# Optimization experiments

Hardware: AMD Instinct MI355X
Metric: run time of the kernel (lower is better)

Reference implementation:

```python
import jax, jax.numpy as jnp
import numpy as np

B, S, D, H, FF, R, NB = 8, 1024, 768, 12, 3072, 16, 768


def _ln(x, g, b, eps=1e-6):
    m = x.mean(-1, keepdims=True)
    v = jnp.mean((x - m) ** 2, axis=-1, keepdims=True)
    return (x - m) * jax.lax.rsqrt(v + eps) * g + b


def setup_inputs() -> dict:
    key = jax.random.key(0)

    def rn(i, shape, s=0.02):
        return jax.random.normal(jax.random.fold_in(key, i), shape, jnp.float32) * s

    inp = {
        "x": jax.random.normal(jax.random.fold_in(key, 0), (B, S, D), jnp.float32),
        "attn_mask": jnp.zeros((S, S), jnp.float32),
        "norm1_g": jnp.ones((D,), jnp.float32),
        "norm1_b": jnp.zeros((D,), jnp.float32),
        "q_w": rn(1, (D, D)), "q_b": jnp.zeros((D,), jnp.float32),
        "k_w": rn(2, (D, D)), "k_b": jnp.zeros((D,), jnp.float32),
        "v_w": rn(3, (D, D)), "v_b": jnp.zeros((D,), jnp.float32),
        "o_w": rn(4, (D, D)), "o_b": jnp.zeros((D,), jnp.float32),
        "norm2_g": jnp.ones((D,), jnp.float32),
        "norm2_b": jnp.zeros((D,), jnp.float32),
        "fc1_w": rn(5, (FF, D)), "fc1_b": jnp.zeros((FF,), jnp.float32),
        "fc2_w": rn(6, (D, FF)), "fc2_b": jnp.zeros((D,), jnp.float32),
        # shared LoRA (backbone tokens)
        "lora1_A": rn(7, (D, R)), "lora1_B": rn(8, (R, FF)),
        "lora2_A": rn(9, (FF, R)), "lora2_B": rn(10, (R, D)),
        # expert VeRA: frozen shared A/B, per-expert diagonal scaling vectors
        "vera1_A": rn(11, (D, R)), "vera1_B": rn(12, (R, FF)),
        "vera2_A": rn(13, (FF, R)), "vera2_B": rn(14, (R, D)),
        "expert_fc1_d": rn(15, (R,), 1.0), "expert_fc1_b": rn(16, (FF,), 1.0),
        "expert_fc2_d": rn(17, (R,), 1.0), "expert_fc2_b": rn(18, (D,), 1.0),
        "num_backbone_tokens": NB,
    }
    return inp


def reference(x, attn_mask, norm1_g, norm1_b, q_w, q_b, k_w, k_b, v_w, v_b,
              o_w, o_b, norm2_g, norm2_b, fc1_w, fc1_b, fc2_w, fc2_b,
              lora1_A, lora1_B, lora2_A, lora2_B,
              vera1_A, vera1_B, vera2_A, vera2_B,
              expert_fc1_d, expert_fc1_b, expert_fc2_d, expert_fc2_b,
              num_backbone_tokens):
    bsz, seq, dim = x.shape
    hd = dim // H                      # head_dim = 64
    scale = hd ** -0.5
    nb = num_backbone_tokens

    # ---- attention (manual bmm + mask + softmax, eval-mode dropout = identity) ----
    h = _ln(x, norm1_g, norm1_b)
    q = (h @ q_w.T + q_b).reshape(bsz, seq, H, hd)
    k = (h @ k_w.T + k_b).reshape(bsz, seq, H, hd)
    v = (h @ v_w.T + v_b).reshape(bsz, seq, H, hd)
    scores = jnp.einsum('bqhd,bkhd->bhqk', q * scale, k) + attn_mask  # [B,H,S,S]
    probs = jax.nn.softmax(scores, axis=-1)
    ao = jnp.einsum('bhqk,bkhd->bqhd', probs, v).reshape(bsz, seq, dim)
    x = x + (ao @ o_w.T + o_b)

    # ---- MLP with split backbone (shared LoRA) / expert (VeRA) adapters ----
    residual = x
    n2 = _ln(x, norm2_g, norm2_b)
    hid = n2 @ fc1_w.T + fc1_b                                   # [B,S,FF]
    hid_b = hid[:, :nb] + (n2[:, :nb] @ lora1_A) @ lora1_B
    hid_e = hid[:, nb:] + (((n2[:, nb:] @ vera1_A) * expert_fc1_d) @ vera1_B) * expert_fc1_b
    hid = jnp.concatenate([hid_b, hid_e], axis=1)
    hid = jax.nn.gelu(hid)
    out = hid @ fc2_w.T + fc2_b                                  # [B,S,D]
    out_b = out[:, :nb] + (hid[:, :nb] @ lora2_A) @ lora2_B
    out_e = out[:, nb:] + (((hid[:, nb:] @ vera2_A) * expert_fc2_d) @ vera2_B) * expert_fc2_b
    out = jnp.concatenate([out_b, out_e], axis=1)
    return residual + out
```

## Files before the change

### kernel.cpp

```cpp
#include <hip/hip_runtime.h>
#include <stdint.h>

#define B_  8
#define S_  1024
#define D_  768
#define H_  12
#define HD_ 64
#define FF_ 3072
#define M_  (B_*S_)
#define R_  16
#define QLD 2304
#define KBLK 128

typedef unsigned short u16;
typedef short s16x8 __attribute__((ext_vector_type(8)));
typedef float fx4  __attribute__((ext_vector_type(4)));

__device__ __forceinline__ float b2f(u16 u) {
  union { unsigned int i; float f; } c; c.i = ((unsigned int)u) << 16; return c.f;
}
__device__ __forceinline__ u16 f2b(float f) {
  union { float f; unsigned int i; } c; c.f = f;
  unsigned int x = c.i;
  x += 0x7FFFu + ((x >> 16) & 1u);
  return (u16)(x >> 16);
}
__device__ __forceinline__ float gelu_f(float x) {
  float u = 0.7978845608028654f * (x + 0.044715f * x * x * x);
  float e = __expf(2.f * u);
  float t = 1.f - 2.f / (e + 1.f);
  return 0.5f * x * (1.f + t);
}
__device__ __forceinline__ void gload16(const u16* gsrc, u16* ldst) {
  __builtin_amdgcn_global_load_lds(
      (__attribute__((address_space(1))) void*)(gsrc),
      (__attribute__((address_space(3))) void*)(ldst), 16, 0, 0);
}

__global__ __launch_bounds__(256)
void cvt_all(const float* __restrict__ q_w, const float* __restrict__ k_w,
             const float* __restrict__ v_w, const float* __restrict__ o_w,
             const float* __restrict__ fc1_w, const float* __restrict__ fc2_w,
             u16* __restrict__ wqkv, u16* __restrict__ wo,
             u16* __restrict__ wfc1, u16* __restrict__ wfc2)
{
  const int i = blockIdx.x * 256 + threadIdx.x;
  const int q1  = D_ * D_ / 4;
  const int fd4 = FF_ * D_ / 4;
  const float* s; u16* d; int j;
  if      (i <     q1)       { s = q_w;   d = wqkv;            j = i; }
  else if (i < 2 * q1)       { s = k_w;   d = wqkv + D_*D_;    j = i - q1; }
  else if (i < 3 * q1)       { s = v_w;   d = wqkv + 2*D_*D_;  j = i - 2*q1; }
  else if (i < 4 * q1)       { s = o_w;   d = wo;              j = i - 3*q1; }
  else if (i < 4 * q1 + fd4) { s = fc1_w; d = wfc1;            j = i - 4*q1; }
  else                       { s = fc2_w; d = wfc2;            j = i - 4*q1 - fd4; }
  const float4 f = ((const float4*)s)[j];
  ushort4 o4; o4.x = f2b(f.x); o4.y = f2b(f.y); o4.z = f2b(f.z); o4.w = f2b(f.w);
  ((ushort4*)d)[j] = o4;
}

__global__ __launch_bounds__(256)
void prep_all(const float* __restrict__ q_bv, const float* __restrict__ k_bv,
              const float* __restrict__ v_bv, float* __restrict__ qkvb,
              const float* __restrict__ lora1B, const float* __restrict__ vera1B,
              const float* __restrict__ e1b, u16* __restrict__ up1L, u16* __restrict__ up1V,
              const float* __restrict__ lora2B, const float* __restrict__ vera2B,
              const float* __restrict__ e2b, u16* __restrict__ up2L, u16* __restrict__ up2V,
              const float* __restrict__ lora2A, const float* __restrict__ vera2A,
              u16* __restrict__ a2tL, u16* __restrict__ a2tV)
{
  const int f = blockIdx.x * 256 + threadIdx.x;
  if (f < QLD)
    qkvb[f] = (f < D_) ? q_bv[f] : (f < 2 * D_) ? k_bv[f - D_] : v_bv[f - 2 * D_];
  {
    const float ev = e1b[f];
    #pragma unroll
    for (int r = 0; r < 16; ++r) {
      up1L[(size_t)f * 32 + r] = f2b(lora1B[(size_t)r * FF_ + f]);
      up1V[(size_t)f * 32 + r] = f2b(vera1B[(size_t)r * FF_ + f] * ev);
      up1L[(size_t)f * 32 + 16 + r] = 0;
      up1V[(size_t)f * 32 + 16 + r] = 0;
    }
  }
  {
    const float4* apl = (const float4*)(lora2A + (size_t)f * 16);
    const float4* apv = (const float4*)(vera2A + (size_t)f * 16);
    #pragma unroll
    for (int q4 = 0; q4 < 4; ++q4) {
      const float4 l4 = apl[q4], v4 = apv[q4];
      a2tL[(size_t)(q4*4+0) * FF_ + f] = f2b(l4.x);
      a2tL[(size_t)(q4*4+1) * FF_ + f] = f2b(l4.y);
      a2tL[(size_t)(q4*4+2) * FF_ + f] = f2b(l4.z);
      a2tL[(size_t)(q4*4+3) * FF_ + f] = f2b(l4.w);
      a2tV[(size_t)(q4*4+0) * FF_ + f] = f2b(v4.x);
      a2tV[(size_t)(q4*4+1) * FF_ + f] = f2b(v4.y);
      a2tV[(size_t)(q4*4+2) * FF_ + f] = f2b(v4.z);
      a2tV[(size_t)(q4*4+3) * FF_ + f] = f2b(v4.w);
    }
  }
  if (f < D_) {
    const float ev = e2b[f];
    #pragma unroll
    for (int r = 0; r < 16; ++r) {
      up2L[(size_t)f * 32 + r] = f2b(lora2B[(size_t)r * D_ + f]);
      up2V[(size_t)f * 32 + r] = f2b(vera2B[(size_t)r * D_ + f] * ev);
      up2L[(size_t)f * 32 + 16 + r] = 0;
      up2V[(size_t)f * 32 + 16 + r] = 0;
    }
  }
}

template<bool ADD>
__global__ __launch_bounds__(256)
void ln_k(const float* __restrict__ x, const u16* __restrict__ add,
          const float* __restrict__ g, const float* __restrict__ beta,
          u16* __restrict__ outb, float* __restrict__ xsum,
          const float* __restrict__ Alora, const float* __restrict__ Avera,
          const float* __restrict__ dvec, u16* __restrict__ tmp1b,
          const int* __restrict__ nbp)
{
  const int row = blockIdx.x;
  const size_t base = (size_t)row * D_;
  float v0[3]; float s = 0.f, sq = 0.f;
  #pragma unroll
  for (int i = 0; i < 3; ++i) {
    const int d = threadIdx.x + i * 256;
    float val = x[base + d];
    if (ADD) { val += b2f(add[base + d]); xsum[base + d] = val; }
    v0[i] = val; s += val; sq += val * val;
  }
  #pragma unroll
  for (int mm = 32; mm >= 1; mm >>= 1) { s += __shfl_xor(s, mm); sq += __shfl_xor(sq, mm); }
  __shared__ float ss[4], s2[4];
  if ((threadIdx.x & 63) == 0) { ss[threadIdx.x >> 6] = s; s2[threadIdx.x >> 6] = sq; }
  __syncthreads();
  s  = ss[0] + ss[1] + ss[2] + ss[3];
  sq = s2[0] + s2[1] + s2[2] + s2[3];
  const float mean = s * (1.f / D_);
  const float var  = sq * (1.f / D_) - mean * mean;
  const float rs   = rsqrtf(var + 1e-6f);
  float nv[3];
  #pragma unroll
  for (int i = 0; i < 3; ++i) {
    const int d = threadIdx.x + i * 256;
    nv[i] = (v0[i] - mean) * rs * g[d] + beta[d];
    outb[base + d] = f2b(nv[i]);
  }

  if (ADD) {
    const int nb = *nbp;
    const bool ex = (row % S_) >= nb;
    const float* Am = ex ? Avera : Alora;
    float p[16];
    #pragma unroll
    for (int r = 0; r < 16; ++r) p[r] = 0.f;
    #pragma unroll
    for (int i = 0; i < 3; ++i) {
      const int d = threadIdx.x + i * 256;
      const float4* ap = (const float4*)(Am + (size_t)d * R_);
      const float4 a0 = ap[0], a1 = ap[1], a2 = ap[2], a3 = ap[3];
      const float vv = nv[i];
      p[0]  += vv * a0.x; p[1]  += vv * a0.y; p[2]  += vv * a0.z; p[3]  += vv * a0.w;
      p[4]  += vv * a1.x; p[5]  += vv * a1.y; p[6]  += vv * a1.z; p[7]  += vv * a1.w;
      p[8]  += vv * a2.x; p[9]  += vv * a2.y; p[10] += vv * a2.z; p[11] += vv * a2.w;
      p[12] += vv * a3.x; p[13] += vv * a3.y; p[14] += vv * a3.z; p[15] += vv * a3.w;
    }
    #pragma unroll
    for (int st = 1; st < 16; st <<= 1)
      #pragma unroll
      for (int r = 0; r < 16; ++r) p[r] += __shfl_xor(p[r], st);
    __shared__ float sred[16][16];
    const int grp = threadIdx.x >> 4;
    if ((threadIdx.x & 15) == 0) {
      #pragma unroll
      for (int r = 0; r < 16; ++r) sred[grp][r] = p[r];
    }
    __syncthreads();
    if (threadIdx.x < 16) {
      float v = 0.f;
      #pragma unroll
      for (int gg = 0; gg < 16; ++gg) v += sred[gg][threadIdx.x];
      if (ex) v *= dvec[threadIdx.x];
      tmp1b[(size_t)row * 32 + threadIdx.x] = f2b(v);
      tmp1b[(size_t)row * 32 + 16 + threadIdx.x] = 0;
    }
  }
}

template<int MODE>
__global__ __launch_bounds__(256)
void gemm_bt(const u16* __restrict__ A, const u16* __restrict__ W,
             const float* __restrict__ bias, u16* __restrict__ Cb,
             float* __restrict__ Cf, const float* __restrict__ resid,
             const u16* __restrict__ Aad, const u16* __restrict__ BadL,
             const u16* __restrict__ BadV, const int* __restrict__ nbp,
             int M, int N, int K)
{
  __shared__ u16 As[2][128 * 32];
  __shared__ u16 Bs[2][128 * 32];
  const int tid   = threadIdx.x;
  const int lane  = tid & 63;
  const int wid   = tid >> 6;
  const int wr    = wid >> 1;
  const int wc    = wid & 1;
  const int lr    = lane & 15;
  const int lk    = (lane >> 4) << 3;
  const int gn    = N >> 7;
  const int nwg   = (M >> 7) * gn;
  const int chunk = nwg >> 3;
  const int lin   = blockIdx.x;
  const int swz   = (lin & 7) * chunk + (lin >> 3);
  const int m0    = (swz / gn) * 128;
  const int n0    = (swz % gn) * 128;
  const int kg    = (tid & 3) * 8;
  const int row_a = tid >> 2;

  const int nst = K >> 5;
  const int tot = (MODE >= 1) ? nst + 1 : nst;
  const u16* Bad = nullptr;
  if (MODE >= 1) Bad = ((m0 % S_) >= *nbp) ? BadV : BadL;

  const u16* arow = A + (size_t)(m0 + row_a) * K + kg;
  const u16* wrow = W + (size_t)(n0 + row_a) * K + kg;
  const size_t half_a = (size_t)64 * K;

  fx4 acc[4][4];
  const fx4 zero = {0.f, 0.f, 0.f, 0.f};
  #pragma unroll
  for (int i = 0; i < 4; ++i)
    #pragma unroll
    for (int j = 0; j < 4; ++j) acc[i][j] = zero;

  gload16(arow,          &As[0][tid * 8]);
  gload16(arow + half_a, &As[0][(256 + tid) * 8]);
  gload16(wrow,          &Bs[0][tid * 8]);
  gload16(wrow + half_a, &Bs[0][(256 + tid) * 8]);
  __syncthreads();

  for (int t = 0; t < tot; ++t) {
    const int cur = t & 1;
    if (t + 1 < tot) {
      const int nxt = cur ^ 1;
      if (MODE >= 1 && t + 1 == nst) {
        gload16(Aad + (size_t)(m0 + row_a) * 32 + kg,      &As[nxt][tid * 8]);
        gload16(Aad + (size_t)(m0 + 64 + row_a) * 32 + kg, &As[nxt][(256 + tid) * 8]);
        gload16(Bad + (size_t)(n0 + row_a) * 32 + kg,      &Bs[nxt][tid * 8]);
        gload16(Bad + (size_t)(n0 + 64 + row_a) * 32 + kg, &Bs[nxt][(256 + tid) * 8]);
      } else {
        const size_t ko = (size_t)(t + 1) * 32;
        gload16(arow + ko,          &As[nxt][tid * 8]);
        gload16(arow + ko + half_a, &As[nxt][(256 + tid) * 8]);
        gload16(wrow + ko,          &Bs[nxt][tid * 8]);
        gload16(wrow + ko + half_a, &Bs[nxt][(256 + tid) * 8]);
      }
    }
    s16x8 av[4], bv[4];
    #pragma unroll
    for (int i = 0; i < 4; ++i)
      av[i] = *(const s16x8*)&As[cur][(wr * 64 + i * 16 + lr) * 32 + lk];
    #pragma unroll
    for (int j = 0; j < 4; ++j)
      bv[j] = *(const s16x8*)&Bs[cur][(wc * 64 + j * 16 + lr) * 32 + lk];
    __builtin_amdgcn_s_setprio(1);
    #pragma unroll
    for (int i = 0; i < 4; ++i)
      #pragma unroll
      for (int j = 0; j < 4; ++j)
        acc[i][j] = __builtin_amdgcn_mfma_f32_16x16x32_bf16(av[i], bv[j], acc[i][j], 0, 0, 0);
    __builtin_amdgcn_s_setprio(0);
    __syncthreads();
  }

  const int rb = (lane >> 4) * 4;
  #pragma unroll
  for (int j = 0; j < 4; ++j) {
    const int col = n0 + wc * 64 + j * 16 + lr;
    const float bj = bias ? bias[col] : 0.f;
    #pragma unroll
    for (int i = 0; i < 4; ++i) {
      const int row = m0 + wr * 64 + i * 16 + rb;
      #pragma unroll
      for (int r = 0; r < 4; ++r) {
        const float val = acc[i][j][r] + bj;
        const size_t idx = (size_t)(row + r) * N + col;
        if (MODE == 1)      Cb[idx] = f2b(gelu_f(val));
        else if (MODE == 2) Cf[idx] = resid[idx] + val;
        else                Cb[idx] = f2b(val);
      }
    }
  }
}

__global__ __launch_bounds__(256)
void downproj(const u16* __restrict__ hid, const u16* __restrict__ A2tL,
              const u16* __restrict__ A2tV, float* __restrict__ part,
              const int* __restrict__ nbp)
{
  __shared__ u16 As[2][128 * 32];
  __shared__ u16 Bs[2][16 * 32];
  const int tid  = threadIdx.x;
  const int lane = tid & 63;
  const int w    = tid >> 6;
  const int lr   = lane & 15;
  const int lk   = (lane >> 4) << 3;
  const int m0   = blockIdx.x * 128;
  const int kb   = blockIdx.y * (FF_ / 8);
  const int nb   = *nbp;
  const u16* A2t = ((m0 % S_) >= nb) ? A2tV : A2tL;
  const int kg    = (tid & 3) * 8;
  const int row_a = tid >> 2;

  const u16* hrow = hid + (size_t)(m0 + row_a) * FF_ + kb + kg;
  const size_t half_h = (size_t)64 * FF_;
  const u16* brow = A2t + (size_t)(tid >> 2) * FF_ + kb + kg;

  const fx4 zero = {0.f, 0.f, 0.f, 0.f};
  fx4 acc[2]; acc[0] = zero; acc[1] = zero;

  const int nst = (FF_ / 8) >> 5;
  gload16(hrow,          &As[0][tid * 8]);
  gload16(hrow + half_h, &As[0][(256 + tid) * 8]);
  if (tid < 64) gload16(brow, &Bs[0][tid * 8]);
  __syncthreads();

  for (int t = 0; t < nst; ++t) {
    const int cur = t & 1;
    if (t + 1 < nst) {
      const int nxt = cur ^ 1;
      const size_t ko = (size_t)(t + 1) * 32;
      gload16(hrow + ko,          &As[nxt][tid * 8]);
      gload16(hrow + ko + half_h, &As[nxt][(256 + tid) * 8]);
      if (tid < 64) gload16(brow + ko, &Bs[nxt][tid * 8]);
    }
    s16x8 bv = *(const s16x8*)&Bs[cur][lr * 32 + lk];
    #pragma unroll
    for (int i = 0; i < 2; ++i) {
      s16x8 av = *(const s16x8*)&As[cur][(w * 32 + i * 16 + lr) * 32 + lk];
      acc[i] = __builtin_amdgcn_mfma_f32_16x16x32_bf16(av, bv, acc[i], 0, 0, 0);
    }
    __syncthreads();
  }

  const int rb = (lane >> 4) * 4;
  #pragma unroll
  for (int i = 0; i < 2; ++i)
    #pragma unroll
    for (int r = 0; r < 4; ++r)
      part[(size_t)blockIdx.y * M_ * 16 +
           (size_t)(m0 + w * 32 + i * 16 + rb + r) * 16 + lr] = acc[i][r];
}

__global__ __launch_bounds__(256)
void reduce_dp(const float* __restrict__ part, const float* __restrict__ d2,
               u16* __restrict__ tmp2b, const int* __restrict__ nbp)
{
  const int idx = blockIdx.x * 256 + threadIdx.x;
  const int m = idx >> 4, r = idx & 15;
  const int nb = *nbp;
  float s = 0.f;
  #pragma unroll
  for (int ks = 0; ks < 8; ++ks) s += part[(size_t)ks * M_ * 16 + idx];
  if ((m % S_) >= nb) s *= d2[r];
  tmp2b[(size_t)m * 32 + r] = f2b(s);
  tmp2b[(size_t)m * 32 + 16 + r] = 0;
}

__global__ __launch_bounds__(256)
void attn_mfma(const u16* __restrict__ qkv, const float* __restrict__ mask,
               u16* __restrict__ o)
{
  __shared__ u16 Kl[2][128 * 64];
  __shared__ u16 Vt[2][64 * 128];
  __shared__ uint32_t Pl[4][1024];

  const int tid  = threadIdx.x;
  const int lane = tid & 63;
  const int wq   = tid >> 6;
  const int lr   = lane & 15;
  const int hi   = lane >> 4;
  const int lin = blockIdx.x;
  const int vsw = (lin & 7) * 192 + (lin >> 3);
  const int qb  = vsw & 15;
  const int bh  = vsw >> 4;
  const int b    = bh / H_;
  const int h    = bh % H_;
  const size_t tok0 = (size_t)b * S_ + (size_t)qb * 64;
  const size_t colh = (size_t)h * HD_;

  const int va  = tid >> 3;
  const int vc8 = (tid & 7) * 8;
  u16* qstage = (u16*)&Pl[0][0];

  #pragma unroll
  for (int u = 0; u < 2; ++u) {
    const int li = u * 256 + tid;
    const int r  = li >> 3;
    const int cb = ((li & 7) ^ (r & 7)) * 8;
    gload16(qkv + (tok0 + r) * QLD + colh + cb, &qstage[li * 8]);
  }
  {
    const size_t ktok = (size_t)b * S_;
    #pragma unroll
    for (int u = 0; u < 4; ++u) {
      const int li = u * 256 + tid;
      const int r  = li >> 3;
      const int cb = ((li & 7) ^ (r & 7)) * 8;
      gload16(qkv + (ktok + r) * QLD + D_ + colh + cb, &Kl[0][li * 8]);
    }
    const u16* vp = qkv + (ktok + 4 * va) * QLD + 2 * D_ + colh + vc8;
    s16x8 w0 = *(const s16x8*)vp;
    s16x8 w1 = *(const s16x8*)(vp + QLD);
    s16x8 w2 = *(const s16x8*)(vp + 2 * QLD);
    s16x8 w3 = *(const s16x8*)(vp + 3 * QLD);
    #pragma unroll
    for (int jj = 0; jj < 8; ++jj) {
      const int d  = vc8 + jj;
      const int sw = ((d & 7) ^ ((d >> 3) & 7)) << 3;
      const int cp = (4 * va) ^ sw;
      *(uint32_t*)&Vt[0][d * 128 + cp] =
          (uint32_t)(u16)w0[jj] | ((uint32_t)(u16)w1[jj] << 16);
      *(uint32_t*)&Vt[0][d * 128 + cp + 2] =
          (uint32_t)(u16)w2[jj] | ((uint32_t)(u16)w3[jj] << 16);
    }
  }
  __syncthreads();

  s16x8 qa[2];
  {
    const int qrow = wq * 16 + lr;
    #pragma unroll
    for (int ks = 0; ks < 2; ++ks)
      qa[ks] = *(const s16x8*)&qstage[qrow * 64 + ((ks * 32 + hi * 8) ^ ((qrow & 7) << 3))];
  }
  __syncthreads();

  const fx4 zero = {0.f, 0.f, 0.f, 0.f};
  fx4 oacc[4];
  #pragma unroll
  for (int dj = 0; dj < 4; ++dj) oacc[dj] = zero;
  float mreg = -3.0e38f, lreg = 0.f;

  const int NT = S_ / KBLK;
  for (int kt = 0; kt < NT; ++kt) {
    const int cur = kt & 1;
    const int nxt = cur ^ 1;

    s16x8 w0, w1, w2, w3;
    if (kt + 1 < NT) {
      const size_t ktokn = (size_t)b * S_ + (size_t)(kt + 1) * KBLK;
      #pragma unroll
      for (int u = 0; u < 4; ++u) {
        const int li = u * 256 + tid;
        const int r  = li >> 3;
        const int cb = ((li & 7) ^ (r & 7)) * 8;
        gload16(qkv + (ktokn + r) * QLD + D_ + colh + cb, &Kl[nxt][li * 8]);
      }
      const u16* vp = qkv + (ktokn + 4 * va) * QLD + 2 * D_ + colh + vc8;
      w0 = *(const s16x8*)vp;
      w1 = *(const s16x8*)(vp + QLD);
      w2 = *(const s16x8*)(vp + 2 * QLD);
      w3 = *(const s16x8*)(vp + 3 * QLD);
    }

    float val[8][4];
    #pragma unroll
    for (int jh = 0; jh < 2; ++jh) {
      s16x8 kb2[4][2];
      #pragma unroll
      for (int j = 0; j < 4; ++j) {
        const int n = (jh * 4 + j) * 16 + lr;
        #pragma unroll
        for (int ks = 0; ks < 2; ++ks)
          kb2[j][ks] = *(const s16x8*)&Kl[cur][n * 64 + ((ks * 32 + hi * 8) ^ ((n & 7) << 3))];
      }
      fx4 m4[4];
      {
        const float* mp = mask + (size_t)(qb * 64 + wq * 16 + lr) * S_
                        + (size_t)kt * KBLK + jh * 64 + 4 * hi;
        #pragma unroll
        for (int j = 0; j < 4; ++j)
          m4[j] = *(const fx4*)(mp + j * 16);
      }
      fx4 sf[4];
      #pragma unroll
      for (int j = 0; j < 4; ++j) sf[j] = zero;
      __builtin_amdgcn_s_setprio(1);
      #pragma unroll
      for (int ks = 0; ks < 2; ++ks)
        #pragma unroll
        for (int j = 0; j < 4; ++j)
          sf[j] = __builtin_amdgcn_mfma_f32_16x16x32_bf16(kb2[j][ks], qa[ks], sf[j], 0, 0, 0);
      __builtin_amdgcn_s_setprio(0);
      #pragma unroll
      for (int j = 0; j < 4; ++j)
        #pragma unroll
        for (int r = 0; r < 4; ++r)
          val[jh * 4 + j][r] = sf[j][r] * 0.125f + m4[j][r];
    }

    {
      float mk[8];
      #pragma unroll
      for (int kg = 0; kg < 8; ++kg)
        mk[kg] = fmaxf(fmaxf(val[kg][0], val[kg][1]), fmaxf(val[kg][2], val[kg][3]));
      float mx = fmaxf(fmaxf(fmaxf(mk[0], mk[1]), fmaxf(mk[2], mk[3])),
                       fmaxf(fmaxf(mk[4], mk[5]), fmaxf(mk[6], mk[7])));
      mx = fmaxf(mx, __shfl_xor(mx, 16));
      mx = fmaxf(mx, __shfl_xor(mx, 32));
      const float mn  = fmaxf(mreg, mx);
      const float fac = __expf(mreg - mn);
      mreg = mn;
      float sk[8];
      #pragma unroll
      for (int kg = 0; kg < 8; ++kg) {
        #pragma unroll
        for (int r = 0; r < 4; ++r) val[kg][r] = __expf(val[kg][r] - mn);
        sk[kg] = (val[kg][0] + val[kg][1]) + (val[kg][2] + val[kg][3]);
      }
      float rs = ((sk[0] + sk[1]) + (sk[2] + sk[3])) + ((sk[4] + sk[5]) + (sk[6] + sk[7]));
      rs += __shfl_xor(rs, 16);
      rs += __shfl_xor(rs, 32);
      lreg = lreg * fac + rs;
      float facr[4];
      #pragma unroll
      for (int r = 0; r < 4; ++r) facr[r] = __shfl(fac, hi * 4 + r);
      #pragma unroll
      for (int dj = 0; dj < 4; ++dj)
        #pragma unroll
        for (int r = 0; r < 4; ++r) oacc[dj][r] *= facr[r];
    }

    {
      uint32_t* prow = &Pl[wq][lr * 64];
      #pragma unroll
      for (int kg = 0; kg < 8; ++kg) {
        const uint32_t p0 = __builtin_amdgcn_perm(
            __float_as_uint(val[kg][1]), __float_as_uint(val[kg][0]), 0x07060302u);
        const uint32_t p1 = __builtin_amdgcn_perm(
            __float_as_uint(val[kg][3]), __float_as_uint(val[kg][2]), 0x07060302u);
        const int i0 = (8 * kg + 2 * hi) ^ ((lr & 7) << 3);
        uint2 pk; pk.x = p0; pk.y = p1;
        *(uint2*)&prow[i0] = pk;
      }
    }

    if (kt + 1 < NT) {
      #pragma unroll
      for (int jj = 0; jj < 8; ++jj) {
        const int d  = vc8 + jj;
        const int sw = ((d & 7) ^ ((d >> 3) & 7)) << 3;
        const int cp = (4 * va) ^ sw;
        *(uint32_t*)&Vt[nxt][d * 128 + cp] =
            (uint32_t)(u16)w0[jj] | ((uint32_t)(u16)w1[jj] << 16);
        *(uint32_t*)&Vt[nxt][d * 128 + cp + 2] =
            (uint32_t)(u16)w2[jj] | ((uint32_t)(u16)w3[jj] << 16);
      }
    }

    #pragma unroll
    for (int ks = 0; ks < 4; ++ks) {
      const int pbase = (16 * ks + 4 * hi) ^ ((lr & 7) << 3);
      s16x8 pa = *(const s16x8*)&Pl[wq][lr * 64 + pbase];
      s16x8 bv2[4];
      #pragma unroll
      for (int dj = 0; dj < 4; ++dj) {
        const int n  = dj * 16 + lr;
        const int sw = ((n & 7) ^ ((n >> 3) & 7)) << 3;
        bv2[dj] = *(const s16x8*)&Vt[cur][n * 128 + ((ks * 32 + hi * 8) ^ sw)];
      }
      __builtin_amdgcn_s_setprio(1);
      #pragma unroll
      for (int dj = 0; dj < 4; ++dj)
        oacc[dj] = __builtin_amdgcn_mfma_f32_16x16x32_bf16(pa, bv2[dj], oacc[dj], 0, 0, 0);
      __builtin_amdgcn_s_setprio(0);
    }

    __syncthreads();
  }

  {
    const float linv = 1.f / lreg;
    float invr[4];
    #pragma unroll
    for (int r = 0; r < 4; ++r) invr[r] = __shfl(linv, hi * 4 + r);
    #pragma unroll
    for (int r = 0; r < 4; ++r) {
      const size_t grow = (tok0 + wq * 16 + hi * 4 + r) * D_ + colh;
      #pragma unroll
      for (int dj = 0; dj < 4; ++dj)
        o[grow + dj * 16 + lr] = f2b(oacc[dj][r] * invr[r]);
    }
  }
}

extern "C" void kernel_launch(void* const* d_in, const int* in_sizes, int n_in,
                              void* d_out, int out_size, void* d_ws, size_t ws_size,
                              hipStream_t stream)
{
  const float* x      = (const float*)d_in[0];
  const float* mask   = (const float*)d_in[1];
  const float* n1g    = (const float*)d_in[2];
  const float* n1b    = (const float*)d_in[3];
  const float* q_w    = (const float*)d_in[4];
  const float* q_bv   = (const float*)d_in[5];
  const float* k_w    = (const float*)d_in[6];
  const float* k_bv   = (const float*)d_in[7];
  const float* v_w    = (const float*)d_in[8];
  const float* v_bv   = (const float*)d_in[9];
  const float* o_w    = (const float*)d_in[10];
  const float* o_bv   = (const float*)d_in[11];
  const float* n2g    = (const float*)d_in[12];
  const float* n2b    = (const float*)d_in[13];
  const float* fc1_w  = (const float*)d_in[14];
  const float* fc1_bv = (const float*)d_in[15];
  const float* fc2_w  = (const float*)d_in[16];
  const float* fc2_bv = (const float*)d_in[17];
  const float* lora1A = (const float*)d_in[18];
  const float* lora1B = (const float*)d_in[19];
  const float* lora2A = (const float*)d_in[20];
  const float* lora2B = (const float*)d_in[21];
  const float* vera1A = (const float*)d_in[22];
  const float* vera1B = (const float*)d_in[23];
  const float* vera2A = (const float*)d_in[24];
  const float* vera2B = (const float*)d_in[25];
  const float* e1d    = (const float*)d_in[26];
  const float* e1b    = (const float*)d_in[27];
  const float* e2d    = (const float*)d_in[28];
  const float* e2b    = (const float*)d_in[29];
  const int*   nbp    = (const int*)d_in[30];

  char* wsb = (char*)d_ws;
  u16* h1    = (u16*)wsb; wsb += (size_t)M_ * D_ * 2;
  u16* qkv   = (u16*)wsb; wsb += (size_t)M_ * QLD * 2;
  u16* attno = (u16*)wsb; wsb += (size_t)M_ * D_ * 2;
  u16* oproj = (u16*)wsb; wsb += (size_t)M_ * D_ * 2;
  u16* n2    = (u16*)wsb; wsb += (size_t)M_ * D_ * 2;
  u16* wqkv  = (u16*)wsb; wsb += (size_t)QLD * D_ * 2;
  u16* wo    = (u16*)wsb; wsb += (size_t)D_ * D_ * 2;
  u16* wfc1  = (u16*)wsb; wsb += (size_t)FF_ * D_ * 2;
  u16* wfc2  = (u16*)wsb; wsb += (size_t)D_ * FF_ * 2;
  u16* tmp1b = (u16*)wsb; wsb += (size_t)M_ * 32 * 2;
  u16* tmp2b = (u16*)wsb; wsb += (size_t)M_ * 32 * 2;
  u16* up1L  = (u16*)wsb; wsb += (size_t)FF_ * 32 * 2;
  u16* up1V  = (u16*)wsb; wsb += (size_t)FF_ * 32 * 2;
  u16* up2L  = (u16*)wsb; wsb += (size_t)D_ * 32 * 2;
  u16* up2V  = (u16*)wsb; wsb += (size_t)D_ * 32 * 2;
  u16* a2tL  = (u16*)wsb; wsb += (size_t)16 * FF_ * 2;
  u16* a2tV  = (u16*)wsb; wsb += (size_t)16 * FF_ * 2;
  float* qkvb = (float*)wsb; wsb += (size_t)QLD * 4;
  float* part = (float*)wsb; wsb += (size_t)8 * M_ * 16 * 4;
  u16* hidb = h1;

  const int totq = (4 * D_ * D_ + 2 * FF_ * D_) / 4;
  cvt_all<<<totq / 256, 256, 0, stream>>>(q_w, k_w, v_w, o_w, fc1_w, fc2_w,
                                          wqkv, wo, wfc1, wfc2);
  prep_all<<<FF_ / 256, 256, 0, stream>>>(q_bv, k_bv, v_bv, qkvb,
                                          lora1B, vera1B, e1b, up1L, up1V,
                                          lora2B, vera2B, e2b, up2L, up2V,
                                          lora2A, vera2A, a2tL, a2tV);

  ln_k<false><<<M_, 256, 0, stream>>>(x, nullptr, n1g, n1b, h1, nullptr,
                                      nullptr, nullptr, nullptr, nullptr, nullptr);
  gemm_bt<0><<<(M_/128) * (QLD/128), 256, 0, stream>>>(
      h1, wqkv, qkvb, qkv, nullptr, nullptr, nullptr, nullptr, nullptr, nullptr,
      M_, QLD, D_);
  attn_mfma<<<(S_/64) * (B_*H_), 256, 0, stream>>>(qkv, mask, attno);
  gemm_bt<0><<<(M_/128) * (D_/128), 256, 0, stream>>>(
      attno, wo, o_bv, oproj, nullptr, nullptr, nullptr, nullptr, nullptr, nullptr,
      M_, D_, D_);

  ln_k<true><<<M_, 256, 0, stream>>>(x, oproj, n2g, n2b, n2, (float*)d_out,
                                     lora1A, vera1A, e1d, tmp1b, nbp);

  gemm_bt<1><<<(M_/128) * (FF_/128), 256, 0, stream>>>(
      n2, wfc1, fc1_bv, hidb, nullptr, nullptr, tmp1b, up1L, up1V, nbp,
      M_, FF_, D_);

  downproj<<<dim3(M_/128, 8), 256, 0, stream>>>(hidb, a2tL, a2tV, part, nbp);
  reduce_dp<<<M_*16/256, 256, 0, stream>>>(part, e2d, tmp2b, nbp);

  gemm_bt<2><<<(M_/128) * (D_/128), 256, 0, stream>>>(
      hidb, wfc2, fc2_bv, nullptr, (float*)d_out, (const float*)d_out,
      tmp2b, up2L, up2V, nbp, M_, D_, FF_);
}
```

Baseline: 369.4 us.

## Enlarge attention query block to 128 with 8 waves and register-shuffled P

Raises the attention kernel to 8 waves per block covering 128 queries, so each K/V tile loaded into LDS is shared by twice as many query rows and per-thread global load work halves. It also drops the per-wave P staging buffer in LDS: probabilities are packed to bf16 with v_cvt_pk_bf16_f32 and rearranged into the MFMA A-operand layout through lane shuffles. The Q staging reuses the second K buffer. In exchange it adds many cross-lane shuffles, changes the rounding of P from truncation to round-to-nearest, and raises register pressure under the 512-thread launch bound.

Measured after the change: 396.9 us. 1.07x slower.

```diff
diff --git a/kernel.cpp b/kernel.cpp
--- a/kernel.cpp
+++ b/kernel.cpp
@@ -11,6 +11,7 @@
 #define R_  16
 #define QLD 2304
 #define KBLK 128
+#define QBLK 128
 
 typedef unsigned short u16;
 typedef short s16x8 __attribute__((ext_vector_type(8)));
@@ -35,6 +36,11 @@
   __builtin_amdgcn_global_load_lds(
       (__attribute__((address_space(1))) void*)(gsrc),
       (__attribute__((address_space(3))) void*)(ldst), 16, 0, 0);
+}
+__device__ __forceinline__ uint32_t cvtpk(float lo, float hi_) {
+  uint32_t r;
+  asm volatile("v_cvt_pk_bf16_f32 %0, %1, %2" : "=v"(r) : "v"(lo), "v"(hi_));
+  return r;
 }
 
 __global__ __launch_bounds__(256)
@@ -365,72 +371,68 @@
   tmp2b[(size_t)m * 32 + 16 + r] = 0;
 }
 
-__global__ __launch_bounds__(256)
+__global__ __launch_bounds__(512, 4)
 void attn_mfma(const u16* __restrict__ qkv, const float* __restrict__ mask,
                u16* __restrict__ o)
 {
-  __shared__ u16 Kl[2][128 * 64];
-  __shared__ u16 Vt[2][64 * 128];
-  __shared__ uint32_t Pl[4][1024];
+  __shared__ u16 Kl[2][KBLK * 64];
+  __shared__ u16 Vt[2][64 * KBLK];
 
   const int tid  = threadIdx.x;
   const int lane = tid & 63;
-  const int wq   = tid >> 6;
+  const int w    = tid >> 6;
   const int lr   = lane & 15;
   const int hi   = lane >> 4;
   const int lin = blockIdx.x;
-  const int vsw = (lin & 7) * 192 + (lin >> 3);
-  const int qb  = vsw & 15;
-  const int bh  = vsw >> 4;
+  const int vsw = (lin & 7) * 96 + (lin >> 3);
+  const int qb  = vsw & 7;
+  const int bh  = vsw >> 3;
   const int b    = bh / H_;
   const int h    = bh % H_;
-  const size_t tok0 = (size_t)b * S_ + (size_t)qb * 64;
+  const size_t tok0 = (size_t)b * S_ + (size_t)qb * QBLK;
   const size_t colh = (size_t)h * HD_;
 
   const int va  = tid >> 3;
   const int vc8 = (tid & 7) * 8;
-  u16* qstage = (u16*)&Pl[0][0];
+  const int SA  = 32 * (hi & 1) + lr;
+  const int SB  = SA + 16;
 
   #pragma unroll
   for (int u = 0; u < 2; ++u) {
-    const int li = u * 256 + tid;
+    const int li = u * 512 + tid;
     const int r  = li >> 3;
     const int cb = ((li & 7) ^ (r & 7)) * 8;
-    gload16(qkv + (tok0 + r) * QLD + colh + cb, &qstage[li * 8]);
+    gload16(qkv + (tok0 + r) * QLD + colh + cb, &Kl[1][li * 8]);
   }
   {
     const size_t ktok = (size_t)b * S_;
     #pragma unroll
-    for (int u = 0; u < 4; ++u) {
-      const int li = u * 256 + tid;
+    for (int u = 0; u < 2; ++u) {
+      const int li = u * 512 + tid;
       const int r  = li >> 3;
       const int cb = ((li & 7) ^ (r & 7)) * 8;
       gload16(qkv + (ktok + r) * QLD + D_ + colh + cb, &Kl[0][li * 8]);
     }
-    const u16* vp = qkv + (ktok + 4 * va) * QLD + 2 * D_ + colh + vc8;
+    const u16* vp = qkv + (ktok + 2 * va) * QLD + 2 * D_ + colh + vc8;
     s16x8 w0 = *(const s16x8*)vp;
     s16x8 w1 = *(const s16x8*)(vp + QLD);
-    s16x8 w2 = *(const s16x8*)(vp + 2 * QLD);
-    s16x8 w3 = *(const s16x8*)(vp + 3 * QLD);
     #pragma unroll
     for (int jj = 0; jj < 8; ++jj) {
       const int d  = vc8 + jj;
       const int sw = ((d & 7) ^ ((d >> 3) & 7)) << 3;
-      const int cp = (4 * va) ^ sw;
-      *(uint32_t*)&Vt[0][d * 128 + cp] =
+      const int cp = (2 * va) ^ sw;
+      *(uint32_t*)&Vt[0][d * KBLK + cp] =
           (uint32_t)(u16)w0[jj] | ((uint32_t)(u16)w1[jj] << 16);
-      *(uint32_t*)&Vt[0][d * 128 + cp + 2] =
-          (uint32_t)(u16)w2[jj] | ((uint32_t)(u16)w3[jj] << 16);
     }
   }
   __syncthreads();
 
   s16x8 qa[2];
   {
-    const int qrow = wq * 16 + lr;
+    const int qrow = w * 16 + lr;
     #pragma unroll
     for (int ks = 0; ks < 2; ++ks)
-      qa[ks] = *(const s16x8*)&qstage[qrow * 64 + ((ks * 32 + hi * 8) ^ ((qrow & 7) << 3))];
+      qa[ks] = *(const s16x8*)&Kl[1][qrow * 64 + ((ks * 32 + hi * 8) ^ ((qrow & 7) << 3))];
   }
   __syncthreads();
 
@@ -445,21 +447,19 @@
     const int cur = kt & 1;
     const int nxt = cur ^ 1;
 
-    s16x8 w0, w1, w2, w3;
+    s16x8 w0, w1;
     if (kt + 1 < NT) {
       const size_t ktokn = (size_t)b * S_ + (size_t)(kt + 1) * KBLK;
       #pragma unroll
-      for (int u = 0; u < 4; ++u) {
-        const int li = u * 256 + tid;
+      for (int u = 0; u < 2; ++u) {
+        const int li = u * 512 + tid;
         const int r  = li >> 3;
         const int cb = ((li & 7) ^ (r & 7)) * 8;
         gload16(qkv + (ktokn + r) * QLD + D_ + colh + cb, &Kl[nxt][li * 8]);
       }
-      const u16* vp = qkv + (ktokn + 4 * va) * QLD + 2 * D_ + colh + vc8;
+      const u16* vp = qkv + (ktokn + 2 * va) * QLD + 2 * D_ + colh + vc8;
       w0 = *(const s16x8*)vp;
       w1 = *(const s16x8*)(vp + QLD);
-      w2 = *(const s16x8*)(vp + 2 * QLD);
-      w3 = *(const s16x8*)(vp + 3 * QLD);
     }
 
     float val[8][4];
@@ -475,7 +475,7 @@
       }
       fx4 m4[4];
       {
-        const float* mp = mask + (size_t)(qb * 64 + wq * 16 + lr) * S_
+        const float* mp = mask + (size_t)(qb * QBLK + w * 16 + lr) * S_
                         + (size_t)kt * KBLK + jh * 64 + 4 * hi;
         #pragma unroll
         for (int j = 0; j < 4; ++j)
@@ -530,18 +530,32 @@
         for (int r = 0; r < 4; ++r) oacc[dj][r] *= facr[r];
     }
 
-    {
-      uint32_t* prow = &Pl[wq][lr * 64];
-      #pragma unroll
-      for (int kg = 0; kg < 8; ++kg) {
-        const uint32_t p0 = __builtin_amdgcn_perm(
-            __float_as_uint(val[kg][1]), __float_as_uint(val[kg][0]), 0x07060302u);
-        const uint32_t p1 = __builtin_amdgcn_perm(
-            __float_as_uint(val[kg][3]), __float_as_uint(val[kg][2]), 0x07060302u);
-        const int i0 = (8 * kg + 2 * hi) ^ ((lr & 7) << 3);
-        uint2 pk; pk.x = p0; pk.y = p1;
-        *(uint2*)&prow[i0] = pk;
-      }
+    uint32_t c[8][2];
+    #pragma unroll
+    for (int kg = 0; kg < 8; ++kg) {
+      c[kg][0] = cvtpk(val[kg][0], val[kg][1]);
+      c[kg][1] = cvtpk(val[kg][2], val[kg][3]);
+    }
+    const bool upk = hi >= 2;
+    s16x8 pa[4];
+    #pragma unroll
+    for (int ks = 0; ks < 4; ++ks) {
+      const uint32_t e0a = (uint32_t)__shfl((int)c[2*ks][0],   SA);
+      const uint32_t e0b = (uint32_t)__shfl((int)c[2*ks+1][0], SA);
+      const uint32_t e1a = (uint32_t)__shfl((int)c[2*ks][1],   SA);
+      const uint32_t e1b_ = (uint32_t)__shfl((int)c[2*ks+1][1], SA);
+      const uint32_t e2a = (uint32_t)__shfl((int)c[2*ks][0],   SB);
+      const uint32_t e2b_ = (uint32_t)__shfl((int)c[2*ks+1][0], SB);
+      const uint32_t e3a = (uint32_t)__shfl((int)c[2*ks][1],   SB);
+      const uint32_t e3b = (uint32_t)__shfl((int)c[2*ks+1][1], SB);
+      uint32_t pv[4];
+      pv[0] = upk ? e0b  : e0a;
+      pv[1] = upk ? e1b_ : e1a;
+      pv[2] = upk ? e2b_ : e2a;
+      pv[3] = upk ? e3b  : e3a;
+      union { uint32_t u[4]; s16x8 v; } cvt;
+      cvt.u[0] = pv[0]; cvt.u[1] = pv[1]; cvt.u[2] = pv[2]; cvt.u[3] = pv[3];
+      pa[ks] = cvt.v;
     }
 
     if (kt + 1 < NT) {
@@ -549,29 +563,25 @@
       for (int jj = 0; jj < 8; ++jj) {
         const int d  = vc8 + jj;
         const int sw = ((d & 7) ^ ((d >> 3) & 7)) << 3;
-        const int cp = (4 * va) ^ sw;
-        *(uint32_t*)&Vt[nxt][d * 128 + cp] =
+        const int cp = (2 * va) ^ sw;
+        *(uint32_t*)&Vt[nxt][d * KBLK + cp] =
             (uint32_t)(u16)w0[jj] | ((uint32_t)(u16)w1[jj] << 16);
-        *(uint32_t*)&Vt[nxt][d * 128 + cp + 2] =
-            (uint32_t)(u16)w2[jj] | ((uint32_t)(u16)w3[jj] << 16);
       }
     }
 
     #pragma unroll
     for (int ks = 0; ks < 4; ++ks) {
-      const int pbase = (16 * ks + 4 * hi) ^ ((lr & 7) << 3);
-      s16x8 pa = *(const s16x8*)&Pl[wq][lr * 64 + pbase];
       s16x8 bv2[4];
       #pragma unroll
       for (int dj = 0; dj < 4; ++dj) {
         const int n  = dj * 16 + lr;
         const int sw = ((n & 7) ^ ((n >> 3) & 7)) << 3;
-        bv2[dj] = *(const s16x8*)&Vt[cur][n * 128 + ((ks * 32 + hi * 8) ^ sw)];
+        bv2[dj] = *(const s16x8*)&Vt[cur][n * KBLK + ((ks * 32 + hi * 8) ^ sw)];
       }
       __builtin_amdgcn_s_setprio(1);
       #pragma unroll
       for (int dj = 0; dj < 4; ++dj)
-        oacc[dj] = __builtin_amdgcn_mfma_f32_16x16x32_bf16(pa, bv2[dj], oacc[dj], 0, 0, 0);
+        oacc[dj] = __builtin_amdgcn_mfma_f32_16x16x32_bf16(pa[ks], bv2[dj], oacc[dj], 0, 0, 0);
       __builtin_amdgcn_s_setprio(0);
     }
 
@@ -585,7 +595,7 @@
     for (int r = 0; r < 4; ++r) invr[r] = __shfl(linv, hi * 4 + r);
     #pragma unroll
     for (int r = 0; r < 4; ++r) {
-      const size_t grow = (tok0 + wq * 16 + hi * 4 + r) * D_ + colh;
+      const size_t grow = (tok0 + w * 16 + hi * 4 + r) * D_ + colh;
       #pragma unroll
       for (int dj = 0; dj < 4; ++dj)
         o[grow + dj * 16 + lr] = f2b(oacc[dj][r] * invr[r]);
@@ -664,7 +674,7 @@
   gemm_bt<0><<<(M_/128) * (QLD/128), 256, 0, stream>>>(
       h1, wqkv, qkvb, qkv, nullptr, nullptr, nullptr, nullptr, nullptr, nullptr,
       M_, QLD, D_);
-  attn_mfma<<<(S_/64) * (B_*H_), 256, 0, stream>>>(qkv, mask, attno);
+  attn_mfma<<<(S_/QBLK) * (B_*H_), 512, 0, stream>>>(qkv, mask, attno);
   gemm_bt<0><<<(M_/128) * (D_/128), 256, 0, stream>>>(
       attno, wo, o_bv, oproj, nullptr, nullptr, nullptr, nullptr, nullptr, nullptr,
       M_, D_, D_);
```

## Load Q/K straight to registers in attention, lazy softmax rescale, fuse prep kernels

Applied to the files above, without the earlier changes.

The attention kernel stops staging Q and K tiles in LDS. Each lane now loads its MFMA fragments directly from global memory, which removes the K LDS buffers, the global-to-LDS copies and one barrier, and frees shared memory for occupancy. Online-softmax rescaling of the accumulator is skipped unless the running max grows by more than 8 in some lane, which saves exps and multiplies but lets exponentials reach up to e^8 before renormalisation. The weight-conversion and adapter-prep kernels are merged into one launch; the trade-off is that K reads become strided, uncoalesced global loads that lean on cache.

After: 425.4 us. 1.15x slower.

```diff
diff --git a/kernel.cpp b/kernel.cpp
--- a/kernel.cpp
+++ b/kernel.cpp
@@ -38,29 +38,12 @@
 }
 
 __global__ __launch_bounds__(256)
-void cvt_all(const float* __restrict__ q_w, const float* __restrict__ k_w,
-             const float* __restrict__ v_w, const float* __restrict__ o_w,
-             const float* __restrict__ fc1_w, const float* __restrict__ fc2_w,
-             u16* __restrict__ wqkv, u16* __restrict__ wo,
-             u16* __restrict__ wfc1, u16* __restrict__ wfc2)
-{
-  const int i = blockIdx.x * 256 + threadIdx.x;
-  const int q1  = D_ * D_ / 4;
-  const int fd4 = FF_ * D_ / 4;
-  const float* s; u16* d; int j;
-  if      (i <     q1)       { s = q_w;   d = wqkv;            j = i; }
-  else if (i < 2 * q1)       { s = k_w;   d = wqkv + D_*D_;    j = i - q1; }
-  else if (i < 3 * q1)       { s = v_w;   d = wqkv + 2*D_*D_;  j = i - 2*q1; }
-  else if (i < 4 * q1)       { s = o_w;   d = wo;              j = i - 3*q1; }
-  else if (i < 4 * q1 + fd4) { s = fc1_w; d = wfc1;            j = i - 4*q1; }
-  else                       { s = fc2_w; d = wfc2;            j = i - 4*q1 - fd4; }
-  const float4 f = ((const float4*)s)[j];
-  ushort4 o4; o4.x = f2b(f.x); o4.y = f2b(f.y); o4.z = f2b(f.z); o4.w = f2b(f.w);
-  ((ushort4*)d)[j] = o4;
-}
-
-__global__ __launch_bounds__(256)
-void prep_all(const float* __restrict__ q_bv, const float* __restrict__ k_bv,
+void cvt_prep(const float* __restrict__ q_w, const float* __restrict__ k_w,
+              const float* __restrict__ v_w, const float* __restrict__ o_w,
+              const float* __restrict__ fc1_w, const float* __restrict__ fc2_w,
+              u16* __restrict__ wqkv, u16* __restrict__ wo,
+              u16* __restrict__ wfc1, u16* __restrict__ wfc2,
+              const float* __restrict__ q_bv, const float* __restrict__ k_bv,
               const float* __restrict__ v_bv, float* __restrict__ qkvb,
               const float* __restrict__ lora1B, const float* __restrict__ vera1B,
               const float* __restrict__ e1b, u16* __restrict__ up1L, u16* __restrict__ up1V,
@@ -69,43 +52,60 @@
               const float* __restrict__ lora2A, const float* __restrict__ vera2A,
               u16* __restrict__ a2tL, u16* __restrict__ a2tV)
 {
-  const int f = blockIdx.x * 256 + threadIdx.x;
-  if (f < QLD)
-    qkvb[f] = (f < D_) ? q_bv[f] : (f < 2 * D_) ? k_bv[f - D_] : v_bv[f - 2 * D_];
+  const int i = blockIdx.x * 256 + threadIdx.x;
+  const int q1  = D_ * D_ / 4;
+  const int fd4 = FF_ * D_ / 4;
   {
-    const float ev = e1b[f];
-    #pragma unroll
-    for (int r = 0; r < 16; ++r) {
-      up1L[(size_t)f * 32 + r] = f2b(lora1B[(size_t)r * FF_ + f]);
-      up1V[(size_t)f * 32 + r] = f2b(vera1B[(size_t)r * FF_ + f] * ev);
-      up1L[(size_t)f * 32 + 16 + r] = 0;
-      up1V[(size_t)f * 32 + 16 + r] = 0;
-    }
-  }
-  {
-    const float4* apl = (const float4*)(lora2A + (size_t)f * 16);
-    const float4* apv = (const float4*)(vera2A + (size_t)f * 16);
-    #pragma unroll
-    for (int q4 = 0; q4 < 4; ++q4) {
-      const float4 l4 = apl[q4], v4 = apv[q4];
-      a2tL[(size_t)(q4*4+0) * FF_ + f] = f2b(l4.x);
-      a2tL[(size_t)(q4*4+1) * FF_ + f] = f2b(l4.y);
-      a2tL[(size_t)(q4*4+2) * FF_ + f] = f2b(l4.z);
-      a2tL[(size_t)(q4*4+3) * FF_ + f] = f2b(l4.w);
-      a2tV[(size_t)(q4*4+0) * FF_ + f] = f2b(v4.x);
-      a2tV[(size_t)(q4*4+1) * FF_ + f] = f2b(v4.y);
-      a2tV[(size_t)(q4*4+2) * FF_ + f] = f2b(v4.z);
-      a2tV[(size_t)(q4*4+3) * FF_ + f] = f2b(v4.w);
-    }
-  }
-  if (f < D_) {
-    const float ev = e2b[f];
-    #pragma unroll
-    for (int r = 0; r < 16; ++r) {
-      up2L[(size_t)f * 32 + r] = f2b(lora2B[(size_t)r * D_ + f]);
-      up2V[(size_t)f * 32 + r] = f2b(vera2B[(size_t)r * D_ + f] * ev);
-      up2L[(size_t)f * 32 + 16 + r] = 0;
-      up2V[(size_t)f * 32 + 16 + r] = 0;
+    const float* s; u16* d; int j;
+    if      (i <     q1)       { s = q_w;   d = wqkv;            j = i; }
+    else if (i < 2 * q1)       { s = k_w;   d = wqkv + D_*D_;    j = i - q1; }
+    else if (i < 3 * q1)       { s = v_w;   d = wqkv + 2*D_*D_;  j = i - 2*q1; }
+    else if (i < 4 * q1)       { s = o_w;   d = wo;              j = i - 3*q1; }
+    else if (i < 4 * q1 + fd4) { s = fc1_w; d = wfc1;            j = i - 4*q1; }
+    else                       { s = fc2_w; d = wfc2;            j = i - 4*q1 - fd4; }
+    const float4 f = ((const float4*)s)[j];
+    ushort4 o4; o4.x = f2b(f.x); o4.y = f2b(f.y); o4.z = f2b(f.z); o4.w = f2b(f.w);
+    ((ushort4*)d)[j] = o4;
+  }
+  if (i < FF_) {
+    const int f = i;
+    if (f < QLD)
+      qkvb[f] = (f < D_) ? q_bv[f] : (f < 2 * D_) ? k_bv[f - D_] : v_bv[f - 2 * D_];
+    {
+      const float ev = e1b[f];
+      #pragma unroll
+      for (int r = 0; r < 16; ++r) {
+        up1L[(size_t)f * 32 + r] = f2b(lora1B[(size_t)r * FF_ + f]);
+        up1V[(size_t)f * 32 + r] = f2b(vera1B[(size_t)r * FF_ + f] * ev);
+        up1L[(size_t)f * 32 + 16 + r] = 0;
+        up1V[(size_t)f * 32 + 16 + r] = 0;
+      }
+    }
+    {
+      const float4* apl = (const float4*)(lora2A + (size_t)f * 16);
+      const float4* apv = (const float4*)(vera2A + (size_t)f * 16);
+      #pragma unroll
+      for (int q4 = 0; q4 < 4; ++q4) {
+        const float4 l4 = apl[q4], v4 = apv[q4];
+        a2tL[(size_t)(q4*4+0) * FF_ + f] = f2b(l4.x);
+        a2tL[(size_t)(q4*4+1) * FF_ + f] = f2b(l4.y);
+        a2tL[(size_t)(q4*4+2) * FF_ + f] = f2b(l4.z);
+        a2tL[(size_t)(q4*4+3) * FF_ + f] = f2b(l4.w);
+        a2tV[(size_t)(q4*4+0) * FF_ + f] = f2b(v4.x);
+        a2tV[(size_t)(q4*4+1) * FF_ + f] = f2b(v4.y);
+        a2tV[(size_t)(q4*4+2) * FF_ + f] = f2b(v4.z);
+        a2tV[(size_t)(q4*4+3) * FF_ + f] = f2b(v4.w);
+      }
+    }
+    if (f < D_) {
+      const float ev = e2b[f];
+      #pragma unroll
+      for (int r = 0; r < 16; ++r) {
+        up2L[(size_t)f * 32 + r] = f2b(lora2B[(size_t)r * D_ + f]);
+        up2V[(size_t)f * 32 + r] = f2b(vera2B[(size_t)r * D_ + f] * ev);
+        up2L[(size_t)f * 32 + 16 + r] = 0;
+        up2V[(size_t)f * 32 + 16 + r] = 0;
+      }
     }
   }
 }
@@ -369,8 +369,7 @@
 void attn_mfma(const u16* __restrict__ qkv, const float* __restrict__ mask,
                u16* __restrict__ o)
 {
-  __shared__ u16 Kl[2][128 * 64];
-  __shared__ u16 Vt[2][64 * 128];
+  __shared__ u16 Vt[2][64 * KBLK];
   __shared__ uint32_t Pl[4][1024];
 
   const int tid  = threadIdx.x;
@@ -389,24 +388,16 @@
 
   const int va  = tid >> 3;
   const int vc8 = (tid & 7) * 8;
-  u16* qstage = (u16*)&Pl[0][0];
-
-  #pragma unroll
-  for (int u = 0; u < 2; ++u) {
-    const int li = u * 256 + tid;
-    const int r  = li >> 3;
-    const int cb = ((li & 7) ^ (r & 7)) * 8;
-    gload16(qkv + (tok0 + r) * QLD + colh + cb, &qstage[li * 8]);
-  }
+
+  s16x8 qa[2];
+  {
+    const u16* qrow = qkv + (tok0 + wq * 16 + lr) * QLD + colh;
+    qa[0] = *(const s16x8*)(qrow + hi * 8);
+    qa[1] = *(const s16x8*)(qrow + 32 + hi * 8);
+  }
+
   {
     const size_t ktok = (size_t)b * S_;
-    #pragma unroll
-    for (int u = 0; u < 4; ++u) {
-      const int li = u * 256 + tid;
-      const int r  = li >> 3;
-      const int cb = ((li & 7) ^ (r & 7)) * 8;
-      gload16(qkv + (ktok + r) * QLD + D_ + colh + cb, &Kl[0][li * 8]);
-    }
     const u16* vp = qkv + (ktok + 4 * va) * QLD + 2 * D_ + colh + vc8;
     s16x8 w0 = *(const s16x8*)vp;
     s16x8 w1 = *(const s16x8*)(vp + QLD);
@@ -417,20 +408,11 @@
       const int d  = vc8 + jj;
       const int sw = ((d & 7) ^ ((d >> 3) & 7)) << 3;
       const int cp = (4 * va) ^ sw;
-      *(uint32_t*)&Vt[0][d * 128 + cp] =
+      *(uint32_t*)&Vt[0][d * KBLK + cp] =
           (uint32_t)(u16)w0[jj] | ((uint32_t)(u16)w1[jj] << 16);
-      *(uint32_t*)&Vt[0][d * 128 + cp + 2] =
+      *(uint32_t*)&Vt[0][d * KBLK + cp + 2] =
           (uint32_t)(u16)w2[jj] | ((uint32_t)(u16)w3[jj] << 16);
     }
-  }
-  __syncthreads();
-
-  s16x8 qa[2];
-  {
-    const int qrow = wq * 16 + lr;
-    #pragma unroll
-    for (int ks = 0; ks < 2; ++ks)
-      qa[ks] = *(const s16x8*)&qstage[qrow * 64 + ((ks * 32 + hi * 8) ^ ((qrow & 7) << 3))];
   }
   __syncthreads();
 
@@ -447,31 +429,24 @@
 
     s16x8 w0, w1, w2, w3;
     if (kt + 1 < NT) {
-      const size_t ktokn = (size_t)b * S_ + (size_t)(kt + 1) * KBLK;
-      #pragma unroll
-      for (int u = 0; u < 4; ++u) {
-        const int li = u * 256 + tid;
-        const int r  = li >> 3;
-        const int cb = ((li & 7) ^ (r & 7)) * 8;
-        gload16(qkv + (ktokn + r) * QLD + D_ + colh + cb, &Kl[nxt][li * 8]);
-      }
-      const u16* vp = qkv + (ktokn + 4 * va) * QLD + 2 * D_ + colh + vc8;
+      const u16* vp = qkv + ((size_t)b * S_ + (size_t)(kt + 1) * KBLK + 4 * va) * QLD
+                    + 2 * D_ + colh + vc8;
       w0 = *(const s16x8*)vp;
       w1 = *(const s16x8*)(vp + QLD);
       w2 = *(const s16x8*)(vp + 2 * QLD);
       w3 = *(const s16x8*)(vp + 3 * QLD);
     }
 
+    const size_t ktok = (size_t)b * S_ + (size_t)kt * KBLK;
     float val[8][4];
     #pragma unroll
     for (int jh = 0; jh < 2; ++jh) {
       s16x8 kb2[4][2];
       #pragma unroll
       for (int j = 0; j < 4; ++j) {
-        const int n = (jh * 4 + j) * 16 + lr;
-        #pragma unroll
-        for (int ks = 0; ks < 2; ++ks)
-          kb2[j][ks] = *(const s16x8*)&Kl[cur][n * 64 + ((ks * 32 + hi * 8) ^ ((n & 7) << 3))];
+        const u16* krow = qkv + (ktok + (jh * 4 + j) * 16 + lr) * QLD + D_ + colh;
+        kb2[j][0] = *(const s16x8*)(krow + hi * 8);
+        kb2[j][1] = *(const s16x8*)(krow + 32 + hi * 8);
       }
       fx4 m4[4];
       {
@@ -507,27 +482,33 @@
                        fmaxf(fmaxf(mk[4], mk[5]), fmaxf(mk[6], mk[7])));
       mx = fmaxf(mx, __shfl_xor(mx, 16));
       mx = fmaxf(mx, __shfl_xor(mx, 32));
-      const float mn  = fmaxf(mreg, mx);
-      const float fac = __expf(mreg - mn);
-      mreg = mn;
+      const bool noresc = (bool)__all(mx <= mreg + 8.f);
+      float fac = 1.f;
+      if (!noresc) {
+        const float mn = fmaxf(mreg, mx);
+        fac = __expf(mreg - mn);
+        mreg = mn;
+      }
       float sk[8];
       #pragma unroll
       for (int kg = 0; kg < 8; ++kg) {
         #pragma unroll
-        for (int r = 0; r < 4; ++r) val[kg][r] = __expf(val[kg][r] - mn);
+        for (int r = 0; r < 4; ++r) val[kg][r] = __expf(val[kg][r] - mreg);
         sk[kg] = (val[kg][0] + val[kg][1]) + (val[kg][2] + val[kg][3]);
       }
       float rs = ((sk[0] + sk[1]) + (sk[2] + sk[3])) + ((sk[4] + sk[5]) + (sk[6] + sk[7]));
       rs += __shfl_xor(rs, 16);
       rs += __shfl_xor(rs, 32);
       lreg = lreg * fac + rs;
-      float facr[4];
-      #pragma unroll
-      for (int r = 0; r < 4; ++r) facr[r] = __shfl(fac, hi * 4 + r);
-      #pragma unroll
-      for (int dj = 0; dj < 4; ++dj)
+      if (!noresc) {
+        float facr[4];
         #pragma unroll
-        for (int r = 0; r < 4; ++r) oacc[dj][r] *= facr[r];
+        for (int r = 0; r < 4; ++r) facr[r] = __shfl(fac, hi * 4 + r);
+        #pragma unroll
+        for (int dj = 0; dj < 4; ++dj)
+          #pragma unroll
+          for (int r = 0; r < 4; ++r) oacc[dj][r] *= facr[r];
+      }
     }
 
     {
@@ -550,9 +531,9 @@
         const int d  = vc8 + jj;
         const int sw = ((d & 7) ^ ((d >> 3) & 7)) << 3;
         const int cp = (4 * va) ^ sw;
-        *(uint32_t*)&Vt[nxt][d * 128 + cp] =
+        *(uint32_t*)&Vt[nxt][d * KBLK + cp] =
             (uint32_t)(u16)w0[jj] | ((uint32_t)(u16)w1[jj] << 16);
-        *(uint32_t*)&Vt[nxt][d * 128 + cp + 2] =
+        *(uint32_t*)&Vt[nxt][d * KBLK + cp + 2] =
             (uint32_t)(u16)w2[jj] | ((uint32_t)(u16)w3[jj] << 16);
       }
     }
@@ -566,7 +547,7 @@
       for (int dj = 0; dj < 4; ++dj) {
         const int n  = dj * 16 + lr;
         const int sw = ((n & 7) ^ ((n >> 3) & 7)) << 3;
-        bv2[dj] = *(const s16x8*)&Vt[cur][n * 128 + ((ks * 32 + hi * 8) ^ sw)];
+        bv2[dj] = *(const s16x8*)&Vt[cur][n * KBLK + ((ks * 32 + hi * 8) ^ sw)];
       }
       __builtin_amdgcn_s_setprio(1);
       #pragma unroll
@@ -652,12 +633,12 @@
   u16* hidb = h1;
 
   const int totq = (4 * D_ * D_ + 2 * FF_ * D_) / 4;
-  cvt_all<<<totq / 256, 256, 0, stream>>>(q_w, k_w, v_w, o_w, fc1_w, fc2_w,
-                                          wqkv, wo, wfc1, wfc2);
-  prep_all<<<FF_ / 256, 256, 0, stream>>>(q_bv, k_bv, v_bv, qkvb,
-                                          lora1B, vera1B, e1b, up1L, up1V,
-                                          lora2B, vera2B, e2b, up2L, up2V,
-                                          lora2A, vera2A, a2tL, a2tV);
+  cvt_prep<<<totq / 256, 256, 0, stream>>>(q_w, k_w, v_w, o_w, fc1_w, fc2_w,
+                                           wqkv, wo, wfc1, wfc2,
+                                           q_bv, k_bv, v_bv, qkvb,
+                                           lora1B, vera1B, e1b, up1L, up1V,
+                                           lora2B, vera2B, e2b, up2L, up2V,
+                                           lora2A, vera2A, a2tL, a2tV);
 
   ln_k<false><<<M_, 256, 0, stream>>>(x, nullptr, n1g, n1b, h1, nullptr,
                                       nullptr, nullptr, nullptr, nullptr, nullptr);
```
